# Kernel tuning notes

Measured on AMD Instinct MI355X. Metric: run time of the kernel, lower is better.

## Reference

```python
import jax, jax.numpy as jnp
import numpy as np

B, D, H, NB = 4096, 2048, 2048, 4
BIN, BOUT = D // NB, H // NB
EPS = 1e-5


def _block_linear(x, W, b):
    # x: [B, nb*bin], W: [nb, bin, bout], b: [nb, bout] -> [B, nb*bout]
    xr = x.reshape(x.shape[0], NB, BIN)
    y = jnp.einsum('bni,nio->bno', xr, W) + b
    return y.reshape(x.shape[0], NB * BOUT)


def setup_inputs() -> dict:
    key = jax.random.key(0)
    ks = jax.random.split(key, 24)
    sW = 1.0 / np.sqrt(BIN)
    sR = 1.0 / np.sqrt(BOUT)
    inp = {
        'x': jax.random.normal(ks[0], (B, D), jnp.float32),
        'h_prev': jax.random.normal(ks[1], (B, H), jnp.float32),
        'c_prev': jax.random.normal(ks[2], (B, H), jnp.float32),
        'ln_g': jnp.ones((D,), jnp.float32),
        'ln_b': jnp.zeros((D,), jnp.float32),
        'conv_w': jax.random.normal(ks[3], (3,), jnp.float32) * 0.5,
        'conv_b': jnp.zeros((), jnp.float32),
    }
    names = ['Wz', 'Wi', 'Wf', 'Wo']
    for j, n in enumerate(names):
        inp[n] = jax.random.normal(ks[4 + j], (NB, BIN, BOUT), jnp.float32) * sW
        inp['b' + n[1]] = jax.random.normal(ks[8 + j], (NB, BOUT), jnp.float32) * sW
    rnames = ['Rz', 'Ri', 'Rf', 'Ro']
    for j, n in enumerate(rnames):
        inp[n] = jax.random.normal(ks[12 + j], (NB, BOUT, BOUT), jnp.float32) * sR
        inp['rb' + n[1]] = jax.random.normal(ks[16 + j], (NB, BOUT), jnp.float32) * sR
    return inp


def reference(x, h_prev, c_prev, ln_g, ln_b, conv_w, conv_b,
              Wz, bz, Wi, bi, Wf, bf, Wo, bo,
              Rz, rbz, Ri, rbi, Rf, rbf, Ro, rbo):
    # LayerNorm over the feature dim
    mu = jnp.mean(x, axis=-1, keepdims=True)
    var = jnp.mean((x - mu) ** 2, axis=-1, keepdims=True)
    x_norm = (x - mu) * jax.lax.rsqrt(var + EPS) * ln_g + ln_b

    # Causal conv1d (kernel 3) along the feature axis, then SiLU
    xp = jnp.pad(x_norm, ((0, 0), (2, 0)))  # left-pad 2 -> causal
    xc = conv_w[0] * xp[:, :D] + conv_w[1] * xp[:, 1:D + 1] + conv_w[2] * xp[:, 2:D + 2] + conv_b
    x_conv = jax.nn.silu(xc)

    z = jnp.tanh(_block_linear(x, Wz, bz) + _block_linear(h_prev, Rz, rbz))
    i = jax.nn.sigmoid(_block_linear(x_conv, Wi, bi) + _block_linear(h_prev, Ri, rbi))
    f = jax.nn.sigmoid(_block_linear(x_conv, Wf, bf) + _block_linear(h_prev, Rf, rbf))
    o = jax.nn.sigmoid(_block_linear(x, Wo, bo) + _block_linear(h_prev, Ro, rbo))

    c_t = f * c_prev + i * z
    h_t = o * jnp.tanh(c_t)
    return (h_t, c_t)
```

## Files before the change

kernel.cpp:

```cpp
#include <hip/hip_runtime.h>
#include <hip/hip_bf16.h>
#include <math.h>

#define BB 4096
#define DD 2048
#define HH 2048

typedef __bf16 bf16x8 __attribute__((ext_vector_type(8)));
typedef float f32x4 __attribute__((ext_vector_type(4)));

__device__ __forceinline__ void async16(const void* g, void* l) {
  __builtin_amdgcn_global_load_lds(
      (const __attribute__((address_space(1))) unsigned int*)g,
      (__attribute__((address_space(3))) unsigned int*)l,
      16, 0, 0);
}

__device__ __forceinline__ float sigmoidf_(float x) {
  return 1.0f / (1.0f + __expf(-x));
}
__device__ __forceinline__ float tanhf_(float x) {
  float t = __expf(-2.0f * fabsf(x));
  return copysignf((1.0f - t) / (1.0f + t), x);
}

__device__ __forceinline__ void store_bf8(__hip_bfloat16* dst, const float* v) {
  union { __hip_bfloat16 b[8]; uint4 u; } p;
#pragma unroll
  for (int e = 0; e < 8; e++) p.b[e] = __float2bfloat16(v[e]);
  *(uint4*)dst = p.u;
}

__global__ __launch_bounds__(256) void prep_all(
    const float* __restrict__ x, const float* __restrict__ h,
    const float* __restrict__ lg, const float* __restrict__ lb,
    const float* __restrict__ cw, const float* __restrict__ cb,
    __hip_bfloat16* __restrict__ xh2, __hip_bfloat16* __restrict__ xc2,
    const float* __restrict__ Wz, const float* __restrict__ Wi,
    const float* __restrict__ Wf, const float* __restrict__ Wo,
    const float* __restrict__ Rz, const float* __restrict__ Ri,
    const float* __restrict__ Rf, const float* __restrict__ Ro,
    __hip_bfloat16* __restrict__ WT2,
    const float* __restrict__ bz, const float* __restrict__ bi,
    const float* __restrict__ bf, const float* __restrict__ bo,
    const float* __restrict__ rbz, const float* __restrict__ rbi,
    const float* __restrict__ rbf, const float* __restrict__ rbo,
    float* __restrict__ bias) {
  __shared__ float smf[4224];
  const int b = blockIdx.x, t = threadIdx.x;

  if (b < 4096) {
    const int r = b, l = t & 63;
    const int mb = r >> 7, rl = r & 127, swz = (rl >> 1) & 3;
    const int n = t >> 6, ktl = (t >> 2) & 15, pc = (t & 3) ^ swz;
    float* red = smf;
    float* edge = smf + 8;
    const float* xr = x + (size_t)r * 2048;
    const float* hr = h + (size_t)r * 2048;
    float4 v0 = ((const float4*)xr)[t * 2];
    float4 v1 = ((const float4*)xr)[t * 2 + 1];
    float vv[8] = {v0.x, v0.y, v0.z, v0.w, v1.x, v1.y, v1.z, v1.w};
    float s = 0.f, s2 = 0.f;
#pragma unroll
    for (int e = 0; e < 8; e++) { s += vv[e]; s2 += vv[e] * vv[e]; }
#pragma unroll
    for (int off = 32; off > 0; off >>= 1) {
      s += __shfl_down(s, off);
      s2 += __shfl_down(s2, off);
    }
    const int w = t >> 6;
    if (l == 0) { red[w] = s; red[4 + w] = s2; }
    __syncthreads();
    const float mu = (red[0] + red[1] + red[2] + red[3]) * (1.0f / 2048.0f);
    const float var = (red[4] + red[5] + red[6] + red[7]) * (1.0f / 2048.0f) - mu * mu;
    const float rs = rsqrtf(var + 1e-5f);

    float4 h0 = ((const float4*)hr)[t * 2];
    float4 h1 = ((const float4*)hr)[t * 2 + 1];
    float hh[8] = {h0.x, h0.y, h0.z, h0.w, h1.x, h1.y, h1.z, h1.w};
    float4 g0 = ((const float4*)lg)[t * 2], g1 = ((const float4*)lg)[t * 2 + 1];
    float4 b0 = ((const float4*)lb)[t * 2], b1 = ((const float4*)lb)[t * 2 + 1];
    float gg[8] = {g0.x, g0.y, g0.z, g0.w, g1.x, g1.y, g1.z, g1.w};
    float bbv[8] = {b0.x, b0.y, b0.z, b0.w, b1.x, b1.y, b1.z, b1.w};
    float fr[8];
#pragma unroll
    for (int e = 0; e < 8; e++) fr[e] = (vv[e] - mu) * rs * gg[e] + bbv[e];

    const size_t bx = ((size_t)(mb * 4 + n) * 32 + ktl) * 512 + rl * 4 + pc;
    const size_t bh = ((size_t)(mb * 4 + n) * 32 + 16 + ktl) * 512 + rl * 4 + pc;
    store_bf8(xh2 + bx * 8, vv);
    store_bf8(xh2 + bh * 8, hh);

    edge[t * 2 + 0] = fr[6]; edge[t * 2 + 1] = fr[7];
    __syncthreads();
    float p6 = __shfl_up(fr[6], 1);
    float p7 = __shfl_up(fr[7], 1);
    if (l == 0) {
      p6 = (t > 0) ? edge[(t - 1) * 2 + 0] : 0.f;
      p7 = (t > 0) ? edge[(t - 1) * 2 + 1] : 0.f;
    }
    const float w0 = cw[0], w1 = cw[1], w2 = cw[2], cbv = cb[0];
    float sc[8];
    {
      float xc0 = w0 * p6 + w1 * p7 + w2 * fr[0] + cbv;
      float xc1 = w0 * p7 + w1 * fr[0] + w2 * fr[1] + cbv;
      sc[0] = xc0 * sigmoidf_(xc0);
      sc[1] = xc1 * sigmoidf_(xc1);
    }
#pragma unroll
    for (int e = 2; e < 8; e++) {
      float xc = w0 * fr[e - 2] + w1 * fr[e - 1] + w2 * fr[e] + cbv;
      sc[e] = xc * sigmoidf_(xc);
    }
    const size_t bc = ((size_t)(mb * 4 + n) * 16 + ktl) * 512 + rl * 4 + pc;
    store_bf8(xc2 + bc * 8, sc);

  } else if (b < 6144) {
    const int flat = b - 4096;
    const int jt = flat & 15;
    const int ksg = (flat >> 4) & 7;
    const int gn = flat >> 7;
    const int g = gn >> 2, nn = gn & 3;
    const float* src;
    if (ksg < 4) src = (g == 0 ? Wz : g == 1 ? Wi : g == 2 ? Wf : Wo);
    else         src = (g == 0 ? Rz : g == 1 ? Ri : g == 2 ? Rf : Ro);
    const int kb = (ksg & 3) * 128;

    {
      const int r8 = t >> 3, c4 = t & 7;
      const float* sp = src + ((size_t)nn * 512 + kb + r8) * 512 + jt * 32 + c4 * 4;
#pragma unroll
      for (int rr = 0; rr < 4; rr++) {
        float4 v = *(const float4*)(sp + (size_t)rr * 32 * 512);
        float* d = smf + (r8 + rr * 32) * 33 + c4 * 4;
        d[0] = v.x; d[1] = v.y; d[2] = v.z; d[3] = v.w;
      }
    }
    __syncthreads();
#pragma unroll
    for (int q = 0; q < 2; q++) {
      int u = t + q * 256;
      int ksl = u >> 7, j = (u >> 2) & 31, pc = u & 3;
      int c = pc ^ ((j >> 1) & 3);
      int krl = ksl * 32 + c * 8;
      float v[8];
#pragma unroll
      for (int e = 0; e < 8; e++) v[e] = smf[(krl + e) * 33 + j];
      size_t gr = ((size_t)(gn * 16 + jt) * 32 + ksg * 4 + ksl) * 128 + j * 4 + pc;
      store_bf8(WT2 + gr * 8, v);
    }

  } else {
    int i = (b - 6144) * 256 + t;
    if (i < 2048) {
      bias[0 * 2048 + i] = bz[i] + rbz[i];
      bias[1 * 2048 + i] = bi[i] + rbi[i];
      bias[2 * 2048 + i] = bf[i] + rbf[i];
      bias[3 * 2048 + i] = bo[i] + rbo[i];
    }
  }
}

__global__ __launch_bounds__(512, 4) void gemm_fused(
    const __hip_bfloat16* __restrict__ xh2, const __hip_bfloat16* __restrict__ xc2,
    const __hip_bfloat16* __restrict__ WT2, const float* __restrict__ bias,
    const float* __restrict__ c_prev, float* __restrict__ out) {
  __shared__ __attribute__((aligned(16))) char smem[65536];
  __hip_bfloat16* zo = (__hip_bfloat16*)smem;

  const int mb = blockIdx.x, jt = blockIdx.y, n = blockIdx.z;
  const int t = threadIdx.x, w = t >> 6, l = t & 63;
  const int pair = w >> 2, mhalf = (w >> 1) & 1, jhalf = w & 1;
  const int lj = l & 15;

  const char* pA = (const char*)xh2 + (size_t)(mb * 4 + n) * 262144 + t * 16;
  const char* pC = (const char*)xc2 + (size_t)(mb * 4 + n) * 131072 + t * 16;
  const char* pB = (const char*)WT2 +
      (size_t)(n * 16 + jt * 2 + ((t >> 8) & 1)) * 65536 + ((t >> 7) & 1) * 2048 + (t & 127) * 16;
  char* dA = smem + t * 16;
  char* dB = smem + 32768 + t * 16;

  const int fo = lj * 64 + (((l >> 4) ^ ((lj >> 1) & 3)) * 16);
  const int g0 = pair ? 1 : 0, g1 = pair ? 2 : 3;

  f32x4 acc[4][2][2] = {};

  for (int ks2 = 0; ks2 < 16; ++ks2) {
    __syncthreads();
    async16(pA, dA);
    async16(pA + 8192, dA + 8192);
    if (ks2 < 8) {
      async16(pC, dA + 16384);
      async16(pC + 8192, dA + 24576);
    }
    async16(pB, dB);
    async16(pB + 4194304, dB + 8192);
    async16(pB + 8388608, dB + 16384);
    async16(pB + 12582912, dB + 24576);
    pA += 16384; pC += 16384; pB += 4096;
    __syncthreads();

    const char* Ab = ((ks2 < 8 && pair) ? smem + 16384 : smem) + mhalf * 4096 + fo;
    const char* Bb = smem + 32768 + jhalf * 4096 + fo;
#pragma unroll
    for (int kh = 0; kh < 2; ++kh) {
      bf16x8 af[4];
#pragma unroll
      for (int s = 0; s < 4; ++s)
        af[s] = *(const bf16x8*)(Ab + kh * 8192 + s * 1024);
#pragma unroll
      for (int sj = 0; sj < 2; ++sj) {
        bf16x8 b0 = *(const bf16x8*)(Bb + g0 * 8192 + kh * 2048 + sj * 1024);
        bf16x8 b1 = *(const bf16x8*)(Bb + g1 * 8192 + kh * 2048 + sj * 1024);
#pragma unroll
        for (int s = 0; s < 4; ++s) {
          acc[s][sj][0] = __builtin_amdgcn_mfma_f32_16x16x32_bf16(af[s], b0, acc[s][sj][0], 0, 0, 0);
          acc[s][sj][1] = __builtin_amdgcn_mfma_f32_16x16x32_bf16(af[s], b1, acc[s][sj][1], 0, 0, 0);
        }
      }
    }
  }

  const int r0 = (l >> 4) * 4;
  const int colb = n * 512 + jt * 64;
  __syncthreads();
  if (pair == 0) {
#pragma unroll
    for (int sj = 0; sj < 2; ++sj) {
      const int jc = jhalf * 32 + sj * 16 + lj;
      const float bz_ = bias[colb + jc];
      const float bo_ = bias[3 * 2048 + colb + jc];
#pragma unroll
      for (int s = 0; s < 4; ++s) {
#pragma unroll
        for (int rr = 0; rr < 4; ++rr) {
          const int rl = mhalf * 64 + s * 16 + r0 + rr;
          zo[rl * 72 + jc] = __float2bfloat16(tanhf_(acc[s][sj][0][rr] + bz_));
          zo[(128 + rl) * 72 + jc] = __float2bfloat16(sigmoidf_(acc[s][sj][1][rr] + bo_));
        }
      }
    }
  }
  __syncthreads();
  if (pair == 1) {
    const size_t HC = (size_t)BB * HH;
#pragma unroll
    for (int sj = 0; sj < 2; ++sj) {
      const int jc = jhalf * 32 + sj * 16 + lj;
      const int col = colb + jc;
      const float bi_ = bias[1 * 2048 + col];
      const float bf_ = bias[2 * 2048 + col];
#pragma unroll
      for (int s = 0; s < 4; ++s) {
#pragma unroll
        for (int rr = 0; rr < 4; ++rr) {
          const int rl = mhalf * 64 + s * 16 + r0 + rr;
          const int row = mb * 128 + rl;
          const float z  = __bfloat162float(zo[rl * 72 + jc]);
          const float og = __bfloat162float(zo[(128 + rl) * 72 + jc]);
          const float ig = sigmoidf_(acc[s][sj][0][rr] + bi_);
          const float fg = sigmoidf_(acc[s][sj][1][rr] + bf_);
          const float cp = c_prev[(size_t)row * 2048 + col];
          const float c = fg * cp + ig * z;
          const float hv = og * tanhf_(c);
          out[(size_t)row * 2048 + col] = hv;
          out[HC + (size_t)row * 2048 + col] = c;
        }
      }
    }
  }
}

extern "C" void kernel_launch(void* const* d_in, const int* in_sizes, int n_in,
                              void* d_out, int out_size, void* d_ws, size_t ws_size,
                              hipStream_t stream) {
  const float* x      = (const float*)d_in[0];
  const float* h_prev = (const float*)d_in[1];
  const float* c_prev = (const float*)d_in[2];
  const float* ln_g   = (const float*)d_in[3];
  const float* ln_b   = (const float*)d_in[4];
  const float* conv_w = (const float*)d_in[5];
  const float* conv_b = (const float*)d_in[6];
  const float* Wz = (const float*)d_in[7];
  const float* bz = (const float*)d_in[8];
  const float* Wi = (const float*)d_in[9];
  const float* bi = (const float*)d_in[10];
  const float* Wf = (const float*)d_in[11];
  const float* bf = (const float*)d_in[12];
  const float* Wo = (const float*)d_in[13];
  const float* bo = (const float*)d_in[14];
  const float* Rz = (const float*)d_in[15];
  const float* rbz = (const float*)d_in[16];
  const float* Ri = (const float*)d_in[17];
  const float* rbi = (const float*)d_in[18];
  const float* Rf = (const float*)d_in[19];
  const float* rbf = (const float*)d_in[20];
  const float* Ro = (const float*)d_in[21];
  const float* rbo = (const float*)d_in[22];
  float* out = (float*)d_out;

  char* ws = (char*)d_ws;
  __hip_bfloat16* xh2 = (__hip_bfloat16*)(ws);
  __hip_bfloat16* xc2 = (__hip_bfloat16*)(ws + 33554432);
  __hip_bfloat16* WT2 = (__hip_bfloat16*)(ws + 33554432 + 16777216);
  float* bias         = (float*)(ws + 33554432 + 2 * 16777216);

  prep_all<<<6152, 256, 0, stream>>>(
      x, h_prev, ln_g, ln_b, conv_w, conv_b, xh2, xc2,
      Wz, Wi, Wf, Wo, Rz, Ri, Rf, Ro, WT2,
      bz, bi, bf, bo, rbz, rbi, rbf, rbo, bias);
  gemm_fused<<<dim3(32, 8, 4), 512, 0, stream>>>(xh2, xc2, WT2, bias, c_prev, out);
}
```

Measured before the change: 321.8 us.

## Process one row per wavefront in prep kernel, drop block-level syncs

The activation-prep branch now assigns one 2048-wide row to a single wavefront, with each lane handling 32 contiguous elements, instead of one row per 256-thread block. LayerNorm statistics use only wave shuffles, and the conv edge values pass between lanes by shuffle and a running carry, so the shared-memory reductions and both __syncthreads are gone. Weight-transpose blocks are placed first in the grid and the grid shrinks to match. Each thread now holds 64 floats in registers, which may lower occupancy, and the per-lane 128-byte strided loads coalesce differently than before.

```diff
diff --git a/kernel.cpp b/kernel.cpp
--- a/kernel.cpp
+++ b/kernel.cpp
@@ -49,74 +49,8 @@
   __shared__ float smf[4224];
   const int b = blockIdx.x, t = threadIdx.x;
 
-  if (b < 4096) {
-    const int r = b, l = t & 63;
-    const int mb = r >> 7, rl = r & 127, swz = (rl >> 1) & 3;
-    const int n = t >> 6, ktl = (t >> 2) & 15, pc = (t & 3) ^ swz;
-    float* red = smf;
-    float* edge = smf + 8;
-    const float* xr = x + (size_t)r * 2048;
-    const float* hr = h + (size_t)r * 2048;
-    float4 v0 = ((const float4*)xr)[t * 2];
-    float4 v1 = ((const float4*)xr)[t * 2 + 1];
-    float vv[8] = {v0.x, v0.y, v0.z, v0.w, v1.x, v1.y, v1.z, v1.w};
-    float s = 0.f, s2 = 0.f;
-#pragma unroll
-    for (int e = 0; e < 8; e++) { s += vv[e]; s2 += vv[e] * vv[e]; }
-#pragma unroll
-    for (int off = 32; off > 0; off >>= 1) {
-      s += __shfl_down(s, off);
-      s2 += __shfl_down(s2, off);
-    }
-    const int w = t >> 6;
-    if (l == 0) { red[w] = s; red[4 + w] = s2; }
-    __syncthreads();
-    const float mu = (red[0] + red[1] + red[2] + red[3]) * (1.0f / 2048.0f);
-    const float var = (red[4] + red[5] + red[6] + red[7]) * (1.0f / 2048.0f) - mu * mu;
-    const float rs = rsqrtf(var + 1e-5f);
-
-    float4 h0 = ((const float4*)hr)[t * 2];
-    float4 h1 = ((const float4*)hr)[t * 2 + 1];
-    float hh[8] = {h0.x, h0.y, h0.z, h0.w, h1.x, h1.y, h1.z, h1.w};
-    float4 g0 = ((const float4*)lg)[t * 2], g1 = ((const float4*)lg)[t * 2 + 1];
-    float4 b0 = ((const float4*)lb)[t * 2], b1 = ((const float4*)lb)[t * 2 + 1];
-    float gg[8] = {g0.x, g0.y, g0.z, g0.w, g1.x, g1.y, g1.z, g1.w};
-    float bbv[8] = {b0.x, b0.y, b0.z, b0.w, b1.x, b1.y, b1.z, b1.w};
-    float fr[8];
-#pragma unroll
-    for (int e = 0; e < 8; e++) fr[e] = (vv[e] - mu) * rs * gg[e] + bbv[e];
-
-    const size_t bx = ((size_t)(mb * 4 + n) * 32 + ktl) * 512 + rl * 4 + pc;
-    const size_t bh = ((size_t)(mb * 4 + n) * 32 + 16 + ktl) * 512 + rl * 4 + pc;
-    store_bf8(xh2 + bx * 8, vv);
-    store_bf8(xh2 + bh * 8, hh);
-
-    edge[t * 2 + 0] = fr[6]; edge[t * 2 + 1] = fr[7];
-    __syncthreads();
-    float p6 = __shfl_up(fr[6], 1);
-    float p7 = __shfl_up(fr[7], 1);
-    if (l == 0) {
-      p6 = (t > 0) ? edge[(t - 1) * 2 + 0] : 0.f;
-      p7 = (t > 0) ? edge[(t - 1) * 2 + 1] : 0.f;
-    }
-    const float w0 = cw[0], w1 = cw[1], w2 = cw[2], cbv = cb[0];
-    float sc[8];
-    {
-      float xc0 = w0 * p6 + w1 * p7 + w2 * fr[0] + cbv;
-      float xc1 = w0 * p7 + w1 * fr[0] + w2 * fr[1] + cbv;
-      sc[0] = xc0 * sigmoidf_(xc0);
-      sc[1] = xc1 * sigmoidf_(xc1);
-    }
-#pragma unroll
-    for (int e = 2; e < 8; e++) {
-      float xc = w0 * fr[e - 2] + w1 * fr[e - 1] + w2 * fr[e] + cbv;
-      sc[e] = xc * sigmoidf_(xc);
-    }
-    const size_t bc = ((size_t)(mb * 4 + n) * 16 + ktl) * 512 + rl * 4 + pc;
-    store_bf8(xc2 + bc * 8, sc);
-
-  } else if (b < 6144) {
-    const int flat = b - 4096;
+  if (b < 2048) {
+    const int flat = b;
     const int jt = flat & 15;
     const int ksg = (flat >> 4) & 7;
     const int gn = flat >> 7;
@@ -150,8 +84,86 @@
       store_bf8(WT2 + gr * 8, v);
     }
 
+  } else if (b < 3072) {
+    const int wid = t >> 6, l = t & 63;
+    const int r = (b - 2048) * 4 + wid;
+    const int mb = r >> 7, rl = r & 127;
+    const int swz = (rl >> 1) & 3;
+    const int n = l >> 4, ktl = l & 15;
+
+    const float* xr = x + (size_t)r * 2048 + l * 32;
+    const float* hr = h + (size_t)r * 2048 + l * 32;
+
+    float xv[32], hv[32];
+#pragma unroll
+    for (int q = 0; q < 8; q++) {
+      float4 v = ((const float4*)xr)[q];
+      xv[q * 4 + 0] = v.x; xv[q * 4 + 1] = v.y;
+      xv[q * 4 + 2] = v.z; xv[q * 4 + 3] = v.w;
+    }
+#pragma unroll
+    for (int q = 0; q < 8; q++) {
+      float4 v = ((const float4*)hr)[q];
+      hv[q * 4 + 0] = v.x; hv[q * 4 + 1] = v.y;
+      hv[q * 4 + 2] = v.z; hv[q * 4 + 3] = v.w;
+    }
+
+    const size_t gbx = ((size_t)(mb * 4 + n) * 32 + ktl) * 512 + rl * 4;
+    const size_t gbh = ((size_t)(mb * 4 + n) * 32 + 16 + ktl) * 512 + rl * 4;
+#pragma unroll
+    for (int c = 0; c < 4; c++) store_bf8(xh2 + (gbx + (c ^ swz)) * 8, &xv[c * 8]);
+#pragma unroll
+    for (int c = 0; c < 4; c++) store_bf8(xh2 + (gbh + (c ^ swz)) * 8, &hv[c * 8]);
+
+    float s = 0.f, s2 = 0.f;
+#pragma unroll
+    for (int e = 0; e < 32; e++) { s += xv[e]; s2 += xv[e] * xv[e]; }
+#pragma unroll
+    for (int off = 32; off > 0; off >>= 1) {
+      s += __shfl_xor(s, off);
+      s2 += __shfl_xor(s2, off);
+    }
+    const float mu = s * (1.0f / 2048.0f);
+    const float var = s2 * (1.0f / 2048.0f) - mu * mu;
+    const float rs = rsqrtf(var + 1e-5f);
+
+    const float* gp = lg + l * 32;
+    const float* bp = lb + l * 32;
+    const float fr30 = (xv[30] - mu) * rs * gp[30] + bp[30];
+    const float fr31 = (xv[31] - mu) * rs * gp[31] + bp[31];
+    float p2 = __shfl_up(fr30, 1);
+    float p1 = __shfl_up(fr31, 1);
+    if (l == 0) { p2 = 0.f; p1 = 0.f; }
+
+    const float w0 = cw[0], w1 = cw[1], w2 = cw[2], cbv = cb[0];
+    const size_t cbase = ((size_t)(mb * 4 + n) * 16 + ktl) * 512 + rl * 4;
+#pragma unroll
+    for (int c = 0; c < 4; c++) {
+      float4 g0v = ((const float4*)gp)[c * 2], g1v = ((const float4*)gp)[c * 2 + 1];
+      float4 b0v = ((const float4*)bp)[c * 2], b1v = ((const float4*)bp)[c * 2 + 1];
+      float gg[8] = {g0v.x, g0v.y, g0v.z, g0v.w, g1v.x, g1v.y, g1v.z, g1v.w};
+      float bbv[8] = {b0v.x, b0v.y, b0v.z, b0v.w, b1v.x, b1v.y, b1v.z, b1v.w};
+      float fr8[8], sc8[8];
+#pragma unroll
+      for (int e = 0; e < 8; e++)
+        fr8[e] = (xv[c * 8 + e] - mu) * rs * gg[e] + bbv[e];
+      {
+        float xc0 = w0 * p2 + w1 * p1 + w2 * fr8[0] + cbv;
+        sc8[0] = xc0 * sigmoidf_(xc0);
+        float xc1 = w0 * p1 + w1 * fr8[0] + w2 * fr8[1] + cbv;
+        sc8[1] = xc1 * sigmoidf_(xc1);
+      }
+#pragma unroll
+      for (int e = 2; e < 8; e++) {
+        float xc = w0 * fr8[e - 2] + w1 * fr8[e - 1] + w2 * fr8[e] + cbv;
+        sc8[e] = xc * sigmoidf_(xc);
+      }
+      p2 = fr8[6]; p1 = fr8[7];
+      store_bf8(xc2 + (cbase + (c ^ swz)) * 8, sc8);
+    }
+
   } else {
-    int i = (b - 6144) * 256 + t;
+    int i = (b - 3072) * 256 + t;
     if (i < 2048) {
       bias[0 * 2048 + i] = bz[i] + rbz[i];
       bias[1 * 2048 + i] = bi[i] + rbi[i];
@@ -305,7 +317,7 @@
   __hip_bfloat16* WT2 = (__hip_bfloat16*)(ws + 33554432 + 16777216);
   float* bias         = (float*)(ws + 33554432 + 2 * 16777216);
 
-  prep_all<<<6152, 256, 0, stream>>>(
+  prep_all<<<3080, 256, 0, stream>>>(
       x, h_prev, ln_g, ln_b, conv_w, conv_b, xh2, xc2,
       Wz, Wi, Wf, Wo, Rz, Ri, Rf, Ro, WT2,
       bz, bi, bf, bo, rbz, rbi, rbf, rbo, bias);
```

Measured after the change: 355.4 us. +10.5%, slower.

## Double-buffer GEMM LDS stages with async prefetch and vmcnt waits

Applied to the files above, without the earlier changes.

Restructures the main GEMM loop from a single-buffered 16-step loop with two full barriers per step into a 32-step double-buffered pipeline. The next half-size K stage is prefetched into the alternate LDS buffer while the current one is computed, using explicit s_waitcnt vmcnt and raw s_barrier. It also adds sched_barrier and s_setprio around the MFMA groups. The aim is to hide global-to-LDS load latency behind matrix math. The cost is more barriers per unit of K and correctness that depends on hand-counted vmcnt values and on the raw barrier sequencing.

```diff
diff --git a/kernel.cpp b/kernel.cpp
--- a/kernel.cpp
+++ b/kernel.cpp
@@ -14,6 +14,11 @@
       (const __attribute__((address_space(1))) unsigned int*)g,
       (__attribute__((address_space(3))) unsigned int*)l,
       16, 0, 0);
+}
+
+template <int N>
+__device__ __forceinline__ void wait_vmcnt() {
+  asm volatile("s_waitcnt vmcnt(%0)" ::"n"(N) : "memory");
 }
 
 __device__ __forceinline__ float sigmoidf_(float x) {
@@ -173,52 +178,92 @@
   const int pair = w >> 2, mhalf = (w >> 1) & 1, jhalf = w & 1;
   const int lj = l & 15;
 
-  const char* pA = (const char*)xh2 + (size_t)(mb * 4 + n) * 262144 + t * 16;
-  const char* pC = (const char*)xc2 + (size_t)(mb * 4 + n) * 131072 + t * 16;
-  const char* pB = (const char*)WT2 +
-      (size_t)(n * 16 + jt * 2 + ((t >> 8) & 1)) * 65536 + ((t >> 7) & 1) * 2048 + (t & 127) * 16;
-  char* dA = smem + t * 16;
-  char* dB = smem + 32768 + t * 16;
+  const char* gA = (const char*)xh2 + (size_t)(mb * 4 + n) * 262144 + t * 16;
+  const char* gC = (const char*)xc2 + (size_t)(mb * 4 + n) * 131072 + t * 16;
+  const int u0 = t, u1 = t + 512;
+  const int bg0 = u0 >> 8, bj0 = (u0 >> 7) & 1, br0 = u0 & 127;
+  const int bg1 = u1 >> 8, bj1 = (u1 >> 7) & 1, br1 = u1 & 127;
+  const char* gB0 = (const char*)WT2 +
+      ((size_t)((bg0 * 4 + n) * 16 + jt * 2 + bj0)) * 65536 + br0 * 16;
+  const char* gB1 = (const char*)WT2 +
+      ((size_t)((bg1 * 4 + n) * 16 + jt * 2 + bj1)) * 65536 + br1 * 16;
+  const int dAo = t * 16;
+  const int dB0 = 16384 + bg0 * 4096 + bj0 * 2048 + br0 * 16;
+  const int dB1 = 16384 + bg1 * 4096 + bj1 * 2048 + br1 * 16;
 
   const int fo = lj * 64 + (((l >> 4) ^ ((lj >> 1) & 3)) * 16);
   const int g0 = pair ? 1 : 0, g1 = pair ? 2 : 3;
 
   f32x4 acc[4][2][2] = {};
 
-  for (int ks2 = 0; ks2 < 16; ++ks2) {
-    __syncthreads();
-    async16(pA, dA);
-    async16(pA + 8192, dA + 8192);
-    if (ks2 < 8) {
-      async16(pC, dA + 16384);
-      async16(pC + 8192, dA + 24576);
-    }
-    async16(pB, dB);
-    async16(pB + 4194304, dB + 8192);
-    async16(pB + 8388608, dB + 16384);
-    async16(pB + 12582912, dB + 24576);
-    pA += 16384; pC += 16384; pB += 4096;
-    __syncthreads();
-
-    const char* Ab = ((ks2 < 8 && pair) ? smem + 16384 : smem) + mhalf * 4096 + fo;
-    const char* Bb = smem + 32768 + jhalf * 4096 + fo;
-#pragma unroll
-    for (int kh = 0; kh < 2; ++kh) {
-      bf16x8 af[4];
-#pragma unroll
-      for (int s = 0; s < 4; ++s)
-        af[s] = *(const bf16x8*)(Ab + kh * 8192 + s * 1024);
-#pragma unroll
-      for (int sj = 0; sj < 2; ++sj) {
-        bf16x8 b0 = *(const bf16x8*)(Bb + g0 * 8192 + kh * 2048 + sj * 1024);
-        bf16x8 b1 = *(const bf16x8*)(Bb + g1 * 8192 + kh * 2048 + sj * 1024);
-#pragma unroll
-        for (int s = 0; s < 4; ++s) {
-          acc[s][sj][0] = __builtin_amdgcn_mfma_f32_16x16x32_bf16(af[s], b0, acc[s][sj][0], 0, 0, 0);
-          acc[s][sj][1] = __builtin_amdgcn_mfma_f32_16x16x32_bf16(af[s], b1, acc[s][sj][1], 0, 0, 0);
-        }
-      }
-    }
+#define BAR() __builtin_amdgcn_s_barrier()
+#define SBZ() __builtin_amdgcn_sched_barrier(0)
+
+#define STAGE(h)                                                               \
+  do {                                                                         \
+    char* nb_ = smem + ((h) & 1) * 32768;                                      \
+    async16(gA + (size_t)(h) * 8192, nb_ + dAo);                               \
+    if ((h) < 16) async16(gC + (size_t)(h) * 8192, nb_ + 8192 + dAo);          \
+    async16(gB0 + (size_t)(h) * 2048, nb_ + dB0);                              \
+    async16(gB1 + (size_t)(h) * 2048, nb_ + dB1);                              \
+  } while (0)
+
+#define MFMA8(sj, B0, B1)                                                      \
+  do {                                                                         \
+    acc[0][sj][0] = __builtin_amdgcn_mfma_f32_16x16x32_bf16(af0, B0, acc[0][sj][0], 0, 0, 0); \
+    acc[1][sj][0] = __builtin_amdgcn_mfma_f32_16x16x32_bf16(af1, B0, acc[1][sj][0], 0, 0, 0); \
+    acc[2][sj][0] = __builtin_amdgcn_mfma_f32_16x16x32_bf16(af2, B0, acc[2][sj][0], 0, 0, 0); \
+    acc[3][sj][0] = __builtin_amdgcn_mfma_f32_16x16x32_bf16(af3, B0, acc[3][sj][0], 0, 0, 0); \
+    acc[0][sj][1] = __builtin_amdgcn_mfma_f32_16x16x32_bf16(af0, B1, acc[0][sj][1], 0, 0, 0); \
+    acc[1][sj][1] = __builtin_amdgcn_mfma_f32_16x16x32_bf16(af1, B1, acc[1][sj][1], 0, 0, 0); \
+    acc[2][sj][1] = __builtin_amdgcn_mfma_f32_16x16x32_bf16(af2, B1, acc[2][sj][1], 0, 0, 0); \
+    acc[3][sj][1] = __builtin_amdgcn_mfma_f32_16x16x32_bf16(af3, B1, acc[3][sj][1], 0, 0, 0); \
+  } while (0)
+
+  STAGE(0);
+
+  for (int ks = 0; ks < 32; ++ks) {
+    const int nxt = ks + 1;
+    if (nxt < 16) {
+      STAGE(nxt);
+      wait_vmcnt<4>();
+    } else if (nxt < 32) {
+      STAGE(nxt);
+      wait_vmcnt<3>();
+    } else {
+      wait_vmcnt<0>();
+    }
+    BAR(); SBZ();
+
+    const char* cb = smem + (ks & 1) * 32768;
+    const char* Ab = ((ks < 16 && pair) ? cb + 8192 : cb) + mhalf * 4096 + fo;
+    const char* Bb = cb + 16384 + jhalf * 2048 + fo;
+
+    bf16x8 af0 = *(const bf16x8*)(Ab);
+    bf16x8 af1 = *(const bf16x8*)(Ab + 1024);
+    bf16x8 af2 = *(const bf16x8*)(Ab + 2048);
+    bf16x8 af3 = *(const bf16x8*)(Ab + 3072);
+    {
+      bf16x8 b00 = *(const bf16x8*)(Bb + g0 * 4096);
+      bf16x8 b10 = *(const bf16x8*)(Bb + g1 * 4096);
+      SBZ();
+      __builtin_amdgcn_s_setprio(1);
+      MFMA8(0, b00, b10);
+      __builtin_amdgcn_s_setprio(0);
+      SBZ();
+    }
+    BAR(); SBZ();
+
+    {
+      bf16x8 b01 = *(const bf16x8*)(Bb + g0 * 4096 + 1024);
+      bf16x8 b11 = *(const bf16x8*)(Bb + g1 * 4096 + 1024);
+      SBZ();
+      __builtin_amdgcn_s_setprio(1);
+      MFMA8(1, b01, b11);
+      __builtin_amdgcn_s_setprio(0);
+      SBZ();
+    }
+    BAR(); SBZ();
   }
 
   const int r0 = (l >> 4) * 4;
```

Result: slower. 329.7 us (+2.5%).
